# Kernel tuning notes

Hardware: AMD Instinct MI355X
Metric: run time of the kernel (lower is better)

The kernel has to match this reference:

```python
import jax, jax.numpy as jnp
import numpy as np

B, L, NV = 16, 512, 64
D = 512
PATCH_LEN, STRIDE, PADDING = 16, 8, 8
N_PATCH = (L - PATCH_LEN) // STRIDE + 2  # 64
PRED = 192
MEM = 8192
TOPK = 8
NHEAD = 4
NORM_CONST = 0.4
HEAD_NF = D * N_PATCH


def _pos_emb(n, d):
    pos = np.arange(n)[:, None].astype(np.float32)
    div = np.exp(np.arange(0, d, 2).astype(np.float32) * (-np.log(10000.0) / d))
    pe = np.zeros((n, d), np.float32)
    pe[:, 0::2] = np.sin(pos * div)
    pe[:, 1::2] = np.cos(pos * div)
    return jnp.asarray(pe)

POS = _pos_emb(N_PATCH, D)


def gelu(x):
    return jax.nn.gelu(x, approximate=False)  # torch nn.GELU default = exact erf


def setup_inputs() -> dict:
    key = jax.random.key(0)
    ks = jax.random.split(key, 16)
    s = lambda i, shape, scale=0.02: jax.random.normal(ks[i], shape, jnp.float32) * scale
    return dict(
        x_enc=jax.random.normal(ks[0], (B, L, NV), jnp.float32),
        W_val=s(1, (PATCH_LEN, D), 0.05),
        mem_bank=s(2, (MEM, D), 1.0),
        W_m1=s(3, (D, 2 * D)), b_m1=jnp.zeros((2 * D,), jnp.float32),
        W_m2=s(4, (2 * D, D)), b_m2=jnp.zeros((D,), jnp.float32),
        W_q=s(5, (D, D)), b_q=jnp.zeros((D,), jnp.float32),
        W_k=s(6, (D, D)), b_k=jnp.zeros((D,), jnp.float32),
        W_v=s(7, (D, D)), b_v=jnp.zeros((D,), jnp.float32),
        W_o=s(8, (D, D)), b_o=jnp.zeros((D,), jnp.float32),
        W_g1=s(9, (2 * D, D)), b_g1=jnp.zeros((D,), jnp.float32),
        W_g2=s(10, (D, 2)), b_g2=jnp.zeros((2,), jnp.float32),
        W_h=s(11, (HEAD_NF, PRED)), b_h=jnp.zeros((PRED,), jnp.float32),
        W_f1=s(12, (PRED, 2 * PRED)), b_f1=jnp.zeros((2 * PRED,), jnp.float32),
        W_f2=s(13, (2 * PRED, PRED)), b_f2=jnp.zeros((PRED,), jnp.float32),
    )


def reference(x_enc, W_val, mem_bank, W_m1, b_m1, W_m2, b_m2,
              W_q, b_q, W_k, b_k, W_v, b_v, W_o, b_o,
              W_g1, b_g1, W_g2, b_g2, W_h, b_h, W_f1, b_f1, W_f2, b_f2):
    # instance normalization over the time axis (means detached in torch)
    means = jax.lax.stop_gradient(jnp.mean(x_enc, axis=1, keepdims=True))
    xc = x_enc - means
    stdev = jnp.sqrt(jnp.var(xc, axis=1, keepdims=True) + 1e-5) / NORM_CONST
    x = xc / stdev                                              # [B, L, NV]

    # patch embedding: replication pad at end, unfold, linear + sinusoidal pos
    xt = jnp.transpose(x, (0, 2, 1))                            # [B, NV, L]
    xt = jnp.concatenate([xt, jnp.repeat(xt[..., -1:], PADDING, axis=-1)], axis=-1)
    win = (jnp.arange(N_PATCH) * STRIDE)[:, None] + jnp.arange(PATCH_LEN)  # [N, P]
    patches = xt[..., win].reshape(B * NV, N_PATCH, PATCH_LEN)  # [BN, N, P]
    emb = patches @ W_val + POS                                 # [BN, N, D]

    # local memory: mean-pooled query -> matmul similarity -> top-k gather -> MLP
    qflat = jnp.mean(emb, axis=1)                               # [BN, D]
    sim = qflat @ mem_bank.T                                    # [BN, MEM]
    _, idx = jax.lax.top_k(sim, TOPK)                           # [BN, K]
    retr = mem_bank[idx]                                        # [BN, K, D]
    h = gelu(retr @ W_m1 + b_m1) @ W_m2 + b_m2
    local = jnp.mean(h, axis=1, keepdims=True) + emb            # [BN, N, D]

    # global memory: multihead self-attention (4 heads, batch_first)
    dh = D // NHEAD
    heads = lambda t: t.reshape(B * NV, N_PATCH, NHEAD, dh).transpose(0, 2, 1, 3)
    q = heads(emb @ W_q + b_q)
    k = heads(emb @ W_k + b_k)
    v = heads(emb @ W_v + b_v)
    att = jax.nn.softmax(jnp.einsum('bhqd,bhkd->bhqk', q, k) / jnp.sqrt(jnp.float32(dh)), axis=-1)
    glob = jnp.einsum('bhqk,bhkd->bhqd', att, v).transpose(0, 2, 1, 3).reshape(B * NV, N_PATCH, D)
    glob = glob @ W_o + b_o                                     # [BN, N, D]

    # gated fusion of local/global memory
    comb = jnp.concatenate([local, glob], axis=-1)              # [BN, N, 2D]
    gate = jax.nn.softmax(gelu(comb @ W_g1 + b_g1) @ W_g2 + b_g2, axis=-1)
    mem = gate[..., 0:1] * local + gate[..., 1:2] * glob        # [BN, N, D]

    # flatten -> memory head -> fusion layer with residual
    flat = mem.reshape(B * NV, HEAD_NF)
    mh = (flat @ W_h + b_h).reshape(B, NV, PRED)
    pred = gelu(gelu(mh @ W_f1 + b_f1) @ W_f2 + b_f2) + mh
    pred = jnp.transpose(pred, (0, 2, 1))                       # [B, PRED, NV]

    # denormalize
    return pred * stdev + means
```

## Files before the change

kernel.cpp:

```cpp
#include <hip/hip_runtime.h>
#include <stdint.h>

#define DEV __device__ __forceinline__

typedef uint16_t u16;
typedef __bf16 bf16x8 __attribute__((ext_vector_type(8)));
typedef float f32x4 __attribute__((ext_vector_type(4)));
typedef u16 u16x8 __attribute__((ext_vector_type(8)));

DEV float bf2f(u16 v) { return __uint_as_float(((uint32_t)v) << 16); }
DEV u16 f2bf(float f) {
  uint32_t u = __float_as_uint(f);
  u += 0x7fffu + ((u >> 16) & 1u);
  return (u16)(u >> 16);
}
DEV float gelu_f(float x) { return 0.5f * x * (1.0f + erff(x * 0.7071067811865475f)); }

DEV void gload_lds16(const u16* g, u16* l) {
  __builtin_amdgcn_global_load_lds(
      (const __attribute__((address_space(1))) void*)g,
      (__attribute__((address_space(3))) void*)l, 16, 0, 0);
}

struct __align__(16) Scratch {
  float POSb[64 * 512];
  float meanv[1024];
  float stdv[1024];
  float mh[1024 * 192];
  int idxB[8192];
  float qflat[1024 * 512];
  float gatel[65536 * 2];
  float bqkv[1536];
  u16 hmeanB[1024 * 512];
  u16 gmeanB[1024 * 1024];
  u16 WqkvT[1536 * 512];
  u16 WoT[512 * 512];
  u16 Wm1T[1024 * 512];
  u16 Wm2T[512 * 1024];
  u16 Wg1T[512 * 1024];
  u16 WhT[256 * 32768];
  u16 memdupB[8192 * 1536];
  u16 embh[65536 * 512];
  u16 qkvb[65536 * 1536];
};
__device__ Scratch g_s;

__global__ __launch_bounds__(256) void zerof_kernel(float* __restrict__ p, int n) {
  int t = blockIdx.x * 256 + threadIdx.x;
  if (t < n) p[t] = 0.f;
}
__global__ __launch_bounds__(256) void zerou_kernel(u16* __restrict__ p, int n) {
  int t = blockIdx.x * 256 + threadIdx.x;
  if (t < n) p[t] = 0;
}
__global__ __launch_bounds__(256) void biasqkv_kernel(const float* __restrict__ bq,
                                                      const float* __restrict__ bk,
                                                      const float* __restrict__ bv,
                                                      float* __restrict__ o) {
  int t = blockIdx.x * 256 + threadIdx.x;
  o[t] = t < 512 ? bq[t] : (t < 1024 ? bk[t - 512] : bv[t - 1024]);
}

__global__ __launch_bounds__(256) void pos_kernel(float* __restrict__ POS) {
  int n = blockIdx.x;
  int i = threadIdx.x;
  float div = expf((float)(2 * i) * (-9.210340371976184f / 512.0f));
  float arg = (float)n * div;
  POS[n * 512 + 2 * i] = sinf(arg);
  POS[n * 512 + 2 * i + 1] = cosf(arg);
}

__global__ __launch_bounds__(256) void stats_kernel(const float* __restrict__ x_enc,
                                                    float* __restrict__ meanv,
                                                    float* __restrict__ stdv) {
  int b = blockIdx.x;
  int v = threadIdx.x & 63;
  int g = threadIdx.x >> 6;
  float s = 0.f, s2 = 0.f;
  for (int l = g; l < 512; l += 4) {
    float x = x_enc[((long)b * 512 + l) * 64 + v];
    s += x; s2 += x * x;
  }
  __shared__ float sh[2][4][64];
  sh[0][g][v] = s; sh[1][g][v] = s2;
  __syncthreads();
  if (g == 0) {
    s = sh[0][0][v] + sh[0][1][v] + sh[0][2][v] + sh[0][3][v];
    s2 = sh[1][0][v] + sh[1][1][v] + sh[1][2][v] + sh[1][3][v];
    float mu = s * (1.f / 512.f);
    float var = s2 * (1.f / 512.f) - mu * mu;
    meanv[b * 64 + v] = mu;
    stdv[b * 64 + v] = sqrtf(var + 1e-5f) * 2.5f;
  }
}

__global__ __launch_bounds__(256) void transpose_kernel(const float* __restrict__ in,
                                                        u16* __restrict__ out, int R, int C) {
  __shared__ u16 t[32][33];
  int bx = blockIdx.x * 32;
  int by = blockIdx.y * 32;
  int tx = threadIdx.x & 31, ty = threadIdx.x >> 5;
  for (int i = ty; i < 32; i += 8) t[i][tx] = f2bf(in[(long)(by + i) * C + bx + tx]);
  __syncthreads();
  for (int i = ty; i < 32; i += 8) out[(long)(bx + i) * R + by + tx] = t[tx][i];
}

__global__ __launch_bounds__(256) void emb_kernel(const float* __restrict__ x_enc,
                                                  const float* __restrict__ W_val,
                                                  const float* __restrict__ POS,
                                                  const float* __restrict__ meanv,
                                                  const float* __restrict__ stdv,
                                                  u16* __restrict__ embh,
                                                  float* __restrict__ qflat) {
  int bn = blockIdx.x;
  int b = bn >> 6, v = bn & 63;
  int tid = threadIdx.x;
  __shared__ __align__(16) float wv[16 * 512];
  __shared__ __align__(16) float pt[64 * 16];
  for (int i = tid; i < 8192; i += 256) wv[i] = W_val[i];
  float mu = meanv[bn];
  float inv = 1.f / stdv[bn];
  for (int i = tid; i < 1024; i += 256) {
    int n = i >> 4, p = i & 15;
    int l = n * 8 + p; if (l > 511) l = 511;
    pt[i] = (x_enc[((long)b * 512 + l) * 64 + v] - mu) * inv;
  }
  __syncthreads();
  float qs0 = 0.f, qs1 = 0.f;
  int d0 = tid, d1 = tid + 256;
  for (int n = 0; n < 64; ++n) {
    float a0 = POS[n * 512 + d0], a1 = POS[n * 512 + d1];
#pragma unroll
    for (int p = 0; p < 16; ++p) {
      float pv = pt[n * 16 + p];
      a0 += pv * wv[p * 512 + d0];
      a1 += pv * wv[p * 512 + d1];
    }
    long base = ((long)bn * 64 + n) * 512;
    embh[base + d0] = f2bf(a0);
    embh[base + d1] = f2bf(a1);
    qs0 += a0; qs1 += a1;
  }
  qflat[(long)bn * 512 + d0] = qs0 * (1.f / 64.f);
  qflat[(long)bn * 512 + d1] = qs1 * (1.f / 64.f);
}

__global__ __launch_bounds__(256) void qsplit_kernel(const float* __restrict__ qflat,
                                                     u16* __restrict__ qsC) {
  int t = blockIdx.x * 256 + threadIdx.x;
  int bn = t >> 6, d8 = (t & 63) * 8;
  const float* src = qflat + (long)bn * 512 + d8;
  u16x8 hi, lo;
#pragma unroll
  for (int z = 0; z < 8; ++z) {
    float q = src[z];
    u16 h = f2bf(q);
    hi[z] = h;
    lo[z] = f2bf(q - bf2f(h));
  }
  long base = (long)bn * 1536 + d8;
  *(u16x8*)(qsC + base) = hi;
  *(u16x8*)(qsC + base + 512) = lo;
  *(u16x8*)(qsC + base + 1024) = hi;
}

__global__ __launch_bounds__(256) void memdup_kernel(const float* __restrict__ mb,
                                                     u16* __restrict__ md) {
  int t = blockIdx.x * 256 + threadIdx.x;
  int n = t >> 6, k8 = (t & 63) * 8;
  const float* src = mb + (long)n * 512 + k8;
  u16x8 hi, lo;
#pragma unroll
  for (int z = 0; z < 8; ++z) {
    float m = src[z];
    u16 h = f2bf(m);
    hi[z] = h;
    lo[z] = f2bf(m - bf2f(h));
  }
  long base = (long)n * 1536 + k8;
  *(u16x8*)(md + base) = hi;
  *(u16x8*)(md + base + 512) = hi;
  *(u16x8*)(md + base + 1024) = lo;
}

template <int EPI>
__global__ __launch_bounds__(256) void gemm_nt(const u16* __restrict__ Ag,
                                               const u16* __restrict__ Bt,
                                               const float* __restrict__ bias,
                                               void* __restrict__ C,
                                               int lda, int ldb, int K, int Nreal, int ldc,
                                               int nT) {
  __shared__ __align__(16) u16 smem[2 * 128 * 64];
  u16* As = smem;
  u16* Bs = smem + 8192;
  const int tid = threadIdx.x;
  const int id = blockIdx.x;
  const int xcd = id & 7;
  const int kk = id >> 3;
  const long bm = (long)((kk / nT) * 8 + xcd) * 128;
  const long bnn = (long)(kk % nT) * 128;
  const long koff = (long)blockIdx.z * K;
  const int lane = tid & 63;
  const int w = tid >> 6;
  const int wm = (w & 1) * 64;
  const int wn = (w >> 1) * 64;
  const int r16 = lane & 15;
  const int q4 = lane >> 4;

  f32x4 acc[4][4] = {};

  const u16* ap[4];
  const u16* bp[4];
  u16* al[4];
  u16* bl[4];
#pragma unroll
  for (int j = 0; j < 4; ++j) {
    int cid = (j * 4 + w) * 64 + lane;
    int r = cid >> 3;
    int g = (cid & 7) ^ (r & 7);
    ap[j] = Ag + (bm + r) * lda + koff + g * 8;
    bp[j] = Bt + (bnn + r) * ldb + koff + g * 8;
    al[j] = As + cid * 8;
    bl[j] = Bs + cid * 8;
  }

  for (int k0 = 0; k0 < K; k0 += 64) {
#pragma unroll
    for (int j = 0; j < 4; ++j) gload_lds16(ap[j] + k0, al[j]);
#pragma unroll
    for (int j = 0; j < 4; ++j) gload_lds16(bp[j] + k0, bl[j]);
    __syncthreads();
#pragma unroll
    for (int sub = 0; sub < 2; ++sub) {
      const int gg = q4 + sub * 4;
      bf16x8 av[4], bv[4];
#pragma unroll
      for (int i = 0; i < 4; ++i) {
        int r = wm + i * 16 + r16;
        av[i] = *reinterpret_cast<const bf16x8*>(As + (r * 8 + (gg ^ (r & 7))) * 8);
      }
#pragma unroll
      for (int j2 = 0; j2 < 4; ++j2) {
        int r = wn + j2 * 16 + r16;
        bv[j2] = *reinterpret_cast<const bf16x8*>(Bs + (r * 8 + (gg ^ (r & 7))) * 8);
      }
#pragma unroll
      for (int i = 0; i < 4; ++i)
#pragma unroll
        for (int j2 = 0; j2 < 4; ++j2)
          acc[i][j2] = __builtin_amdgcn_mfma_f32_16x16x32_bf16(av[i], bv[j2], acc[i][j2], 0, 0, 0);
    }
    __syncthreads();
  }

  if (EPI == 2) {
#pragma unroll
    for (int i = 0; i < 4; ++i)
#pragma unroll
      for (int j = 0; j < 4; ++j)
#pragma unroll
        for (int r = 0; r < 4; ++r) {
          long grow = bm + wm + i * 16 + q4 * 4 + r;
          int gcol = (int)bnn + wn + j * 16 + r16;
          if (gcol < Nreal) atomicAdd((float*)C + grow * ldc + gcol, acc[i][j][r]);
        }
  } else if (EPI == 3) {
    float* epf = (float*)smem + w * 2048;
#pragma unroll
    for (int half = 0; half < 2; ++half) {
#pragma unroll
      for (int i = 0; i < 2; ++i)
#pragma unroll
        for (int j = 0; j < 4; ++j)
#pragma unroll
          for (int r = 0; r < 4; ++r)
            epf[(i * 16 + q4 * 4 + r) * 64 + j * 16 + r16] = acc[half * 2 + i][j][r];
      __syncthreads();
#pragma unroll
      for (int v2 = 0; v2 < 8; ++v2) {
        int idx = v2 * 64 + lane;
        int row = idx >> 4, c4 = (idx & 15) * 4;
        f32x4 vec = *(const f32x4*)(epf + row * 64 + c4);
        long grow = bm + wm + half * 32 + row;
        int gcol = (int)bnn + wn + c4;
        if (gcol < Nreal) *(f32x4*)((float*)C + grow * (long)ldc + gcol) = vec;
      }
      __syncthreads();
    }
  } else {
    u16* ep = smem + w * 4096;
    float bcol[4];
#pragma unroll
    for (int j = 0; j < 4; ++j) bcol[j] = bias[bnn + wn + j * 16 + r16];
#pragma unroll
    for (int i = 0; i < 4; ++i)
#pragma unroll
      for (int j = 0; j < 4; ++j)
#pragma unroll
        for (int r = 0; r < 4; ++r) {
          float v = acc[i][j][r] + bcol[j];
          if (EPI == 1) v = gelu_f(v);
          ep[(i * 16 + q4 * 4 + r) * 64 + j * 16 + r16] = f2bf(v);
        }
    __syncthreads();
#pragma unroll
    for (int v2 = 0; v2 < 8; ++v2) {
      int row = v2 * 8 + (lane >> 3);
      int c8 = (lane & 7) * 8;
      u16x8 vec = *(const u16x8*)(ep + row * 64 + c8);
      long grow = bm + wm + row;
      int gcol = (int)bnn + wn + c8;
      if (gcol < Nreal) *(u16x8*)((u16*)C + grow * (long)ldc + gcol) = vec;
    }
  }
}

DEV bool better(float v1, int i1, float v2, int i2) {
  return v1 > v2 || (v1 == v2 && i1 < i2);
}
__global__ __launch_bounds__(256) void topk_kernel(const float* __restrict__ sim,
                                                   int* __restrict__ idxout) {
  const int bn = blockIdx.x;
  const int tid = threadIdx.x;
  const float* row = sim + (long)bn * 8192;
  float bv[8]; int bi[8];
#pragma unroll
  for (int r = 0; r < 8; ++r) { bv[r] = -3.0e38f; bi[r] = 0x7fffffff; }
  for (int n = tid; n < 8192; n += 256) {
    float v = row[n];
    if (better(v, n, bv[7], bi[7])) {
      bv[7] = v; bi[7] = n;
      for (int r = 7; r > 0; --r) {
        if (!better(bv[r], bi[r], bv[r - 1], bi[r - 1])) break;
        float tv = bv[r]; bv[r] = bv[r - 1]; bv[r - 1] = tv;
        int ti = bi[r]; bi[r] = bi[r - 1]; bi[r - 1] = ti;
      }
    }
  }
  __shared__ float lv[256 * 8];
  __shared__ int li[256 * 8];
#pragma unroll
  for (int r = 0; r < 8; ++r) { lv[tid * 8 + r] = bv[r]; li[tid * 8 + r] = bi[r]; }
  __syncthreads();
  for (int step = 128; step >= 1; step >>= 1) {
    if (tid < step) {
      float av[8], xv[8]; int ai[8], xi[8];
#pragma unroll
      for (int r = 0; r < 8; ++r) {
        av[r] = lv[tid * 8 + r]; ai[r] = li[tid * 8 + r];
        xv[r] = lv[(tid + step) * 8 + r]; xi[r] = li[(tid + step) * 8 + r];
      }
      int ia = 0, ib = 0;
      float mv[8]; int mi[8];
#pragma unroll
      for (int r = 0; r < 8; ++r) {
        if (better(av[ia], ai[ia], xv[ib], xi[ib])) { mv[r] = av[ia]; mi[r] = ai[ia]; ++ia; }
        else { mv[r] = xv[ib]; mi[r] = xi[ib]; ++ib; }
      }
#pragma unroll
      for (int r = 0; r < 8; ++r) { lv[tid * 8 + r] = mv[r]; li[tid * 8 + r] = mi[r]; }
    }
    __syncthreads();
  }
  if (tid < 8) idxout[bn * 8 + tid] = li[tid];
}

__global__ __launch_bounds__(256) void gather_kernel(const float* __restrict__ mb,
                                                     const int* __restrict__ idx,
                                                     u16* __restrict__ retrB) {
  int t = blockIdx.x * 256 + threadIdx.x;
  int m = t >> 6;
  int c8 = (t & 63) * 8;
  long r = idx[m];
  if (r < 0) r = 0;
  if (r > 8191) r = 8191;
  const float* src = mb + r * 512 + c8;
  u16x8 o;
#pragma unroll
  for (int z = 0; z < 8; ++z) o[z] = f2bf(src[z]);
  *(u16x8*)(retrB + (long)m * 512 + c8) = o;
}

__global__ __launch_bounds__(256) void gmean_kernel(const u16* __restrict__ hid,
                                                    u16* __restrict__ gmeanB) {
  int t = blockIdx.x * 256 + threadIdx.x;
  int bn = t >> 7, j8 = (t & 127) * 8;
  float s[8] = {};
#pragma unroll
  for (int k = 0; k < 8; ++k) {
    u16x8 v = *(const u16x8*)(hid + (long)(bn * 8 + k) * 1024 + j8);
#pragma unroll
    for (int z = 0; z < 8; ++z) s[z] += bf2f(v[z]);
  }
  u16x8 o;
#pragma unroll
  for (int z = 0; z < 8; ++z) o[z] = f2bf(s[z] * 0.125f);
  *(u16x8*)(gmeanB + (long)bn * 1024 + j8) = o;
}

__global__ __launch_bounds__(256) void attn_kernel(u16* __restrict__ qkvb) {
  __shared__ __align__(16) u16 smem[26752];
  u16* Qs = smem;
  u16* Ks = smem + 8704;
  float* ss = (float*)(smem + 8704);
  u16* ps = smem;
  u16* Vb = smem + 17408;
  float* red = (float*)(smem + 25728);
  const int bn = blockIdx.x, h = blockIdx.y;
  const int tid = threadIdx.x;
  const int lane = tid & 63, w = tid >> 6;
  const int r16 = lane & 15, q4 = lane >> 4;
  const long base = (long)bn * 64 * 1536 + h * 128;

  for (int c = tid; c < 1024; c += 256) {
    int r = c >> 4, c8 = (c & 15) * 8;
    u16x8 vq = *(const u16x8*)(qkvb + base + (long)r * 1536 + c8);
    u16x8 vk = *(const u16x8*)(qkvb + base + (long)r * 1536 + 512 + c8);
    u16x8 vv = *(const u16x8*)(qkvb + base + (long)r * 1536 + 1024 + c8);
    *(u16x8*)(Qs + r * 136 + c8) = vq;
    *(u16x8*)(Ks + r * 136 + c8) = vk;
    int kt = r >> 5, q4t = (r >> 3) & 3, e = r & 7;
    int nt = c8 >> 4, rb = c8 & 15;
    int vbase = (nt * 2 + kt) * 520 + (q4t * 16 + rb) * 8 + e;
#pragma unroll
    for (int z = 0; z < 8; ++z) Vb[vbase + z * 8] = vv[z];
  }
  __syncthreads();

  const int m0 = w * 16;
  f32x4 accS[4] = {};
#pragma unroll
  for (int k0 = 0; k0 < 128; k0 += 32) {
    bf16x8 av = *(const bf16x8*)(Qs + (m0 + r16) * 136 + k0 + q4 * 8);
#pragma unroll
    for (int j = 0; j < 4; ++j) {
      bf16x8 bvf = *(const bf16x8*)(Ks + (j * 16 + r16) * 136 + k0 + q4 * 8);
      accS[j] = __builtin_amdgcn_mfma_f32_16x16x32_bf16(av, bvf, accS[j], 0, 0, 0);
    }
  }
  __syncthreads();
  const float scale = 0.08838834764831845f;
#pragma unroll
  for (int j = 0; j < 4; ++j)
#pragma unroll
    for (int r = 0; r < 4; ++r)
      ss[(m0 + q4 * 4 + r) * 66 + j * 16 + r16] = accS[j][r] * scale;
  __syncthreads();

  {
    int r = tid >> 2, p = tid & 3;
    float* row = ss + r * 66 + p * 16;
    float mx = -3.0e38f;
#pragma unroll
    for (int c2 = 0; c2 < 16; ++c2) mx = fmaxf(mx, row[c2]);
    red[r * 4 + p] = mx;
    __syncthreads();
    float m4 = fmaxf(fmaxf(red[r * 4], red[r * 4 + 1]),
                     fmaxf(red[r * 4 + 2], red[r * 4 + 3]));
    float s = 0.f;
#pragma unroll
    for (int c2 = 0; c2 < 16; ++c2) {
      float e = expf(row[c2] - m4);
      row[c2] = e;
      s += e;
    }
    red[256 + r * 4 + p] = s;
    __syncthreads();
    float inv = 1.f / (red[256 + r * 4] + red[256 + r * 4 + 1] +
                       red[256 + r * 4 + 2] + red[256 + r * 4 + 3]);
    u16x8 o0, o1;
#pragma unroll
    for (int z = 0; z < 8; ++z) {
      o0[z] = f2bf(row[z] * inv);
      o1[z] = f2bf(row[8 + z] * inv);
    }
    *(u16x8*)(ps + r * 72 + p * 16) = o0;
    *(u16x8*)(ps + r * 72 + p * 16 + 8) = o1;
  }
  __syncthreads();

  bf16x8 av0 = *(const bf16x8*)(ps + (m0 + r16) * 72 + q4 * 8);
  bf16x8 av1 = *(const bf16x8*)(ps + (m0 + r16) * 72 + 32 + q4 * 8);
#pragma unroll
  for (int nt = 0; nt < 8; ++nt) {
    f32x4 accO = {};
    bf16x8 bv0 = *(const bf16x8*)(Vb + (nt * 2 + 0) * 520 + lane * 8);
    bf16x8 bv1 = *(const bf16x8*)(Vb + (nt * 2 + 1) * 520 + lane * 8);
    accO = __builtin_amdgcn_mfma_f32_16x16x32_bf16(av0, bv0, accO, 0, 0, 0);
    accO = __builtin_amdgcn_mfma_f32_16x16x32_bf16(av1, bv1, accO, 0, 0, 0);
    int d = nt * 16 + r16;
#pragma unroll
    for (int r = 0; r < 4; ++r) {
      int i = m0 + q4 * 4 + r;
      qkvb[base + (long)i * 1536 + d] = f2bf(accO[r]);
    }
  }
}

__global__ __launch_bounds__(256) void local_kernel(u16* __restrict__ embh,
                                                    const u16* __restrict__ hmeanB) {
  long t = (long)blockIdx.x * 256 + threadIdx.x;
  long e8 = t * 8;
  long m = e8 >> 9;
  int d = (int)(e8 & 511);
  int bn = (int)(m >> 6);
  u16x8 a = *(const u16x8*)(embh + e8);
  u16x8 b = *(const u16x8*)(hmeanB + (long)bn * 512 + d);
  u16x8 o;
#pragma unroll
  for (int z = 0; z < 8; ++z) o[z] = f2bf(bf2f(a[z]) + bf2f(b[z]));
  *(u16x8*)(embh + e8) = o;
}

__global__ __launch_bounds__(256) void gemm_cat(const u16* __restrict__ A1,
                                                const u16* __restrict__ A2,
                                                const u16* __restrict__ Bt,
                                                const float* __restrict__ bias,
                                                const float* __restrict__ W_g2,
                                                float* __restrict__ gatel,
                                                int lda1, int lda2, int nT) {
  __shared__ __align__(16) u16 smem[2 * 128 * 64];
  u16* As = smem;
  u16* Bs = smem + 8192;
  const int tid = threadIdx.x;
  const int id = blockIdx.x;
  const int xcd = id & 7;
  const int kk = id >> 3;
  const long bm = (long)((kk / nT) * 8 + xcd) * 128;
  const long bnn = (long)(kk % nT) * 128;
  const int lane = tid & 63;
  const int w = tid >> 6;
  const int wm = (w & 1) * 64;
  const int wn = (w >> 1) * 64;
  const int r16 = lane & 15;
  const int q4 = lane >> 4;

  f32x4 acc[4][4] = {};

  const u16* ap1[4];
  const u16* ap2[4];
  const u16* bp[4];
  u16* al[4];
  u16* bl[4];
#pragma unroll
  for (int j = 0; j < 4; ++j) {
    int cid = (j * 4 + w) * 64 + lane;
    int r = cid >> 3;
    int g = (cid & 7) ^ (r & 7);
    ap1[j] = A1 + (bm + r) * lda1 + g * 8;
    ap2[j] = A2 + (bm + r) * lda2 + g * 8;
    bp[j] = Bt + (bnn + r) * 1024 + g * 8;
    al[j] = As + cid * 8;
    bl[j] = Bs + cid * 8;
  }

  for (int k0 = 0; k0 < 1024; k0 += 64) {
    if (k0 < 512) {
#pragma unroll
      for (int j = 0; j < 4; ++j) gload_lds16(ap1[j] + k0, al[j]);
    } else {
#pragma unroll
      for (int j = 0; j < 4; ++j) gload_lds16(ap2[j] + (k0 - 512), al[j]);
    }
#pragma unroll
    for (int j = 0; j < 4; ++j) gload_lds16(bp[j] + k0, bl[j]);
    __syncthreads();
#pragma unroll
    for (int sub = 0; sub < 2; ++sub) {
      const int gg = q4 + sub * 4;
      bf16x8 av[4], bv[4];
#pragma unroll
      for (int i = 0; i < 4; ++i) {
        int r = wm + i * 16 + r16;
        av[i] = *reinterpret_cast<const bf16x8*>(As + (r * 8 + (gg ^ (r & 7))) * 8);
      }
#pragma unroll
      for (int j2 = 0; j2 < 4; ++j2) {
        int r = wn + j2 * 16 + r16;
        bv[j2] = *reinterpret_cast<const bf16x8*>(Bs + (r * 8 + (gg ^ (r & 7))) * 8);
      }
#pragma unroll
      for (int i = 0; i < 4; ++i)
#pragma unroll
        for (int j2 = 0; j2 < 4; ++j2)
          acc[i][j2] = __builtin_amdgcn_mfma_f32_16x16x32_bf16(av[i], bv[j2], acc[i][j2], 0, 0, 0);
    }
    __syncthreads();
  }

  float bcol[4], w0[4], w1[4];
#pragma unroll
  for (int j = 0; j < 4; ++j) {
    int gc = (int)bnn + wn + j * 16 + r16;
    bcol[j] = bias[gc];
    w0[j] = W_g2[gc * 2];
    w1[j] = W_g2[gc * 2 + 1];
  }
#pragma unroll
  for (int i = 0; i < 4; ++i)
#pragma unroll
    for (int r = 0; r < 4; ++r) {
      float a0 = 0.f, a1 = 0.f;
#pragma unroll
      for (int j = 0; j < 4; ++j) {
        float h = gelu_f(acc[i][j][r] + bcol[j]);
        a0 += h * w0[j];
        a1 += h * w1[j];
      }
#pragma unroll
      for (int off = 1; off < 16; off <<= 1) {
        a0 += __shfl_xor(a0, off);
        a1 += __shfl_xor(a1, off);
      }
      if (r16 == 0) {
        long row = bm + wm + i * 16 + q4 * 4 + r;
        atomicAdd(&gatel[row * 2], a0);
        atomicAdd(&gatel[row * 2 + 1], a1);
      }
    }
}

__global__ __launch_bounds__(256) void memc_kernel(u16* __restrict__ embh,
                                                   const u16* __restrict__ qkvb,
                                                   const float* __restrict__ gatel,
                                                   const float* __restrict__ b_g2) {
  long t = (long)blockIdx.x * 256 + threadIdx.x;
  long e8 = t * 8;
  long m = e8 >> 9;
  int d = (int)(e8 & 511);
  float l0 = gatel[m * 2] + b_g2[0];
  float l1 = gatel[m * 2 + 1] + b_g2[1];
  float mx = fmaxf(l0, l1);
  float e0 = expf(l0 - mx), e1 = expf(l1 - mx);
  float inv = 1.f / (e0 + e1);
  float g0 = e0 * inv, g1 = e1 * inv;
  u16x8 loc = *(const u16x8*)(embh + e8);
  u16x8 gl = *(const u16x8*)(qkvb + m * 1536 + 512 + d);
  u16x8 o;
#pragma unroll
  for (int z = 0; z < 8; ++z) o[z] = f2bf(g0 * bf2f(loc[z]) + g1 * bf2f(gl[z]));
  *(u16x8*)(embh + e8) = o;
}

__global__ __launch_bounds__(256) void fusion_kernel(const float* __restrict__ mh,
                                                     const float* __restrict__ b_h,
                                                     const float* __restrict__ W_f1,
                                                     const float* __restrict__ b_f1,
                                                     const float* __restrict__ W_f2,
                                                     const float* __restrict__ b_f2,
                                                     const float* __restrict__ meanv,
                                                     const float* __restrict__ stdv,
                                                     float* __restrict__ out) {
  int bn = blockIdx.x;
  int tid = threadIdx.x;
  __shared__ float mrow[192];
  __shared__ float h1[384];
  if (tid < 192) mrow[tid] = mh[(long)bn * 192 + tid] + b_h[tid];
  __syncthreads();
  for (int j = tid; j < 384; j += 256) {
    float a = b_f1[j];
    for (int i = 0; i < 192; ++i) a += mrow[i] * W_f1[i * 384 + j];
    h1[j] = gelu_f(a);
  }
  __syncthreads();
  if (tid < 192) {
    float a = b_f2[tid];
    for (int j = 0; j < 384; ++j) a += h1[j] * W_f2[j * 192 + tid];
    float o = gelu_f(a) + mrow[tid];
    int b = bn >> 6, v = bn & 63;
    out[((long)b * 192 + tid) * 64 + v] = o * stdv[bn] + meanv[bn];
  }
}

extern "C" void kernel_launch(void* const* d_in, const int* in_sizes, int n_in,
                              void* d_out, int out_size, void* d_ws, size_t ws_size,
                              hipStream_t stream) {
  (void)in_sizes; (void)n_in; (void)out_size; (void)d_ws; (void)ws_size;
  const float* x_enc = (const float*)d_in[0];
  const float* W_val = (const float*)d_in[1];
  const float* mem_bank = (const float*)d_in[2];
  const float* W_m1 = (const float*)d_in[3];
  const float* b_m1 = (const float*)d_in[4];
  const float* W_m2 = (const float*)d_in[5];
  const float* b_m2 = (const float*)d_in[6];
  const float* W_q = (const float*)d_in[7];
  const float* b_q = (const float*)d_in[8];
  const float* W_k = (const float*)d_in[9];
  const float* b_k = (const float*)d_in[10];
  const float* W_v = (const float*)d_in[11];
  const float* b_v = (const float*)d_in[12];
  const float* W_o = (const float*)d_in[13];
  const float* b_o = (const float*)d_in[14];
  const float* W_g1 = (const float*)d_in[15];
  const float* b_g1 = (const float*)d_in[16];
  const float* W_g2 = (const float*)d_in[17];
  const float* b_g2 = (const float*)d_in[18];
  const float* W_h = (const float*)d_in[19];
  const float* b_h = (const float*)d_in[20];
  const float* W_f1 = (const float*)d_in[21];
  const float* b_f1 = (const float*)d_in[22];
  const float* W_f2 = (const float*)d_in[23];
  const float* b_f2 = (const float*)d_in[24];

  void* sp = nullptr;
  hipGetSymbolAddress(&sp, HIP_SYMBOL(g_s));
  Scratch* S = (Scratch*)sp;
  float* simB = (float*)S->qkvb;
  u16* qsC = S->qkvb + (size_t)16 * 1024 * 1024;
  u16* retrB = S->qkvb + (size_t)18 * 1024 * 1024;
  u16* hiddenB = S->qkvb + (size_t)24 * 1024 * 1024;

  pos_kernel<<<64, 256, 0, stream>>>(S->POSb);
  stats_kernel<<<16, 256, 0, stream>>>(x_enc, S->meanv, S->stdv);
  zerof_kernel<<<768, 256, 0, stream>>>(S->mh, 1024 * 192);
  zerof_kernel<<<512, 256, 0, stream>>>(S->gatel, 65536 * 2);
  zerou_kernel<<<8192, 256, 0, stream>>>(S->WhT + (size_t)192 * 32768, 64 * 32768);
  biasqkv_kernel<<<6, 256, 0, stream>>>(b_q, b_k, b_v, S->bqkv);
  transpose_kernel<<<dim3(16, 16), 256, 0, stream>>>(W_q, S->WqkvT, 512, 512);
  transpose_kernel<<<dim3(16, 16), 256, 0, stream>>>(W_k, S->WqkvT + 512 * 512, 512, 512);
  transpose_kernel<<<dim3(16, 16), 256, 0, stream>>>(W_v, S->WqkvT + 2 * 512 * 512, 512, 512);
  transpose_kernel<<<dim3(16, 16), 256, 0, stream>>>(W_o, S->WoT, 512, 512);
  transpose_kernel<<<dim3(32, 16), 256, 0, stream>>>(W_m1, S->Wm1T, 512, 1024);
  transpose_kernel<<<dim3(16, 32), 256, 0, stream>>>(W_m2, S->Wm2T, 1024, 512);
  transpose_kernel<<<dim3(16, 32), 256, 0, stream>>>(W_g1, S->Wg1T, 1024, 512);
  transpose_kernel<<<dim3(6, 1024), 256, 0, stream>>>(W_h, S->WhT, 32768, 192);
  memdup_kernel<<<2048, 256, 0, stream>>>(mem_bank, S->memdupB);

  emb_kernel<<<1024, 256, 0, stream>>>(x_enc, W_val, S->POSb, S->meanv, S->stdv,
                                       S->embh, S->qflat);
  qsplit_kernel<<<256, 256, 0, stream>>>(S->qflat, qsC);
  gemm_nt<3><<<512, 256, 0, stream>>>(qsC, S->memdupB, nullptr, simB,
                                      1536, 1536, 1536, 8192, 8192, 64);
  topk_kernel<<<1024, 256, 0, stream>>>(simB, S->idxB);
  gather_kernel<<<2048, 256, 0, stream>>>(mem_bank, S->idxB, retrB);
  gemm_nt<1><<<512, 256, 0, stream>>>(retrB, S->Wm1T, b_m1, hiddenB,
                                      512, 512, 512, 1024, 1024, 8);
  gmean_kernel<<<512, 256, 0, stream>>>(hiddenB, S->gmeanB);
  gemm_nt<0><<<32, 256, 0, stream>>>(S->gmeanB, S->Wm2T, b_m2, S->hmeanB,
                                     1024, 1024, 1024, 512, 512, 4);
  gemm_nt<0><<<6144, 256, 0, stream>>>(S->embh, S->WqkvT, S->bqkv, S->qkvb,
                                       512, 512, 512, 1536, 1536, 12);
  local_kernel<<<16384, 256, 0, stream>>>(S->embh, S->hmeanB);
  attn_kernel<<<dim3(1024, 4), 256, 0, stream>>>(S->qkvb);
  gemm_nt<0><<<2048, 256, 0, stream>>>(S->qkvb, S->WoT, b_o, S->qkvb + 512,
                                       1536, 512, 512, 512, 1536, 4);
  gemm_cat<<<2048, 256, 0, stream>>>(S->embh, S->qkvb + 512, S->Wg1T, b_g1,
                                     W_g2, S->gatel, 512, 1536, 4);
  memc_kernel<<<16384, 256, 0, stream>>>(S->embh, S->qkvb, S->gatel, b_g2);
  gemm_nt<2><<<dim3(16, 1, 16), 256, 0, stream>>>(S->embh, S->WhT, nullptr, S->mh,
                                                  32768, 32768, 2048, 192, 192, 2);
  fusion_kernel<<<1024, 256, 0, stream>>>(S->mh, b_h, W_f1, b_f1, W_f2, b_f2,
                                          S->meanv, S->stdv, (float*)d_out);
}
```

Before: 985.7 us.

## Replace split-K atomics with partial buffers, swizzle epilogue LDS, coalesce attention output

The head GEMM's split-K reduction moves off float atomicAdd. Each of the 16 K-slices now writes its own partial buffer (reusing qkvb scratch), and the fusion kernel sums the 16 partials. This also drops the zeroing of mh. GEMM epilogue LDS staging gets an XOR swizzle to avoid bank conflicts, attention output is staged through LDS so global stores are coalesced 16-byte writes, and the WhT zero-fill kernel is vectorised. Costs are extra partial-buffer traffic and added syncs in attention.

```diff
diff --git a/kernel.cpp b/kernel.cpp
--- a/kernel.cpp
+++ b/kernel.cpp
@@ -49,9 +49,9 @@
   int t = blockIdx.x * 256 + threadIdx.x;
   if (t < n) p[t] = 0.f;
 }
-__global__ __launch_bounds__(256) void zerou_kernel(u16* __restrict__ p, int n) {
+__global__ __launch_bounds__(256) void zerou8_kernel(u16* __restrict__ p, int n8) {
   int t = blockIdx.x * 256 + threadIdx.x;
-  if (t < n) p[t] = 0;
+  if (t < n8) *(u16x8*)(p + (long)t * 8) = (u16x8)0;
 }
 __global__ __launch_bounds__(256) void biasqkv_kernel(const float* __restrict__ bq,
                                                       const float* __restrict__ bk,
@@ -189,7 +189,7 @@
                                                const float* __restrict__ bias,
                                                void* __restrict__ C,
                                                int lda, int ldb, int K, int Nreal, int ldc,
-                                               int nT) {
+                                               int nT, long zstride) {
   __shared__ __align__(16) u16 smem[2 * 128 * 64];
   u16* As = smem;
   u16* Bs = smem + 8192;
@@ -253,18 +253,8 @@
     __syncthreads();
   }
 
-  if (EPI == 2) {
-#pragma unroll
-    for (int i = 0; i < 4; ++i)
-#pragma unroll
-      for (int j = 0; j < 4; ++j)
-#pragma unroll
-        for (int r = 0; r < 4; ++r) {
-          long grow = bm + wm + i * 16 + q4 * 4 + r;
-          int gcol = (int)bnn + wn + j * 16 + r16;
-          if (gcol < Nreal) atomicAdd((float*)C + grow * ldc + gcol, acc[i][j][r]);
-        }
-  } else if (EPI == 3) {
+  if (EPI == 3) {
+    float* Cz = (float*)C + (long)blockIdx.z * zstride;
     float* epf = (float*)smem + w * 2048;
 #pragma unroll
     for (int half = 0; half < 2; ++half) {
@@ -274,16 +264,18 @@
         for (int j = 0; j < 4; ++j)
 #pragma unroll
           for (int r = 0; r < 4; ++r)
-            epf[(i * 16 + q4 * 4 + r) * 64 + j * 16 + r16] = acc[half * 2 + i][j][r];
+            epf[(i * 16 + q4 * 4 + r) * 64 + ((j * 16 + r16) ^ (q4 << 4))] =
+                acc[half * 2 + i][j][r];
       __syncthreads();
 #pragma unroll
       for (int v2 = 0; v2 < 8; ++v2) {
         int idx = v2 * 64 + lane;
         int row = idx >> 4, c4 = (idx & 15) * 4;
-        f32x4 vec = *(const f32x4*)(epf + row * 64 + c4);
+        int c4s = c4 ^ (((row >> 2) & 3) << 4);
+        f32x4 vec = *(const f32x4*)(epf + row * 64 + c4s);
         long grow = bm + wm + half * 32 + row;
         int gcol = (int)bnn + wn + c4;
-        if (gcol < Nreal) *(f32x4*)((float*)C + grow * (long)ldc + gcol) = vec;
+        if (gcol < Nreal) *(f32x4*)(Cz + grow * (long)ldc + gcol) = vec;
       }
       __syncthreads();
     }
@@ -300,14 +292,15 @@
         for (int r = 0; r < 4; ++r) {
           float v = acc[i][j][r] + bcol[j];
           if (EPI == 1) v = gelu_f(v);
-          ep[(i * 16 + q4 * 4 + r) * 64 + j * 16 + r16] = f2bf(v);
+          ep[(i * 16 + q4 * 4 + r) * 64 + ((j * 16 + r16) ^ (q4 << 4))] = f2bf(v);
         }
     __syncthreads();
 #pragma unroll
     for (int v2 = 0; v2 < 8; ++v2) {
       int row = v2 * 8 + (lane >> 3);
       int c8 = (lane & 7) * 8;
-      u16x8 vec = *(const u16x8*)(ep + row * 64 + c8);
+      int c8s = c8 ^ (((row >> 2) & 3) << 4);
+      u16x8 vec = *(const u16x8*)(ep + row * 64 + c8s);
       long grow = bm + wm + row;
       int gcol = (int)bnn + wn + c8;
       if (gcol < Nreal) *(u16x8*)((u16*)C + grow * (long)ldc + gcol) = vec;
@@ -404,6 +397,7 @@
   u16* Ks = smem + 8704;
   float* ss = (float*)(smem + 8704);
   u16* ps = smem;
+  u16* Os = smem;
   u16* Vb = smem + 17408;
   float* red = (float*)(smem + 25728);
   const int bn = blockIdx.x, h = blockIdx.y;
@@ -481,6 +475,7 @@
 
   bf16x8 av0 = *(const bf16x8*)(ps + (m0 + r16) * 72 + q4 * 8);
   bf16x8 av1 = *(const bf16x8*)(ps + (m0 + r16) * 72 + 32 + q4 * 8);
+  __syncthreads();
 #pragma unroll
   for (int nt = 0; nt < 8; ++nt) {
     f32x4 accO = {};
@@ -488,12 +483,21 @@
     bf16x8 bv1 = *(const bf16x8*)(Vb + (nt * 2 + 1) * 520 + lane * 8);
     accO = __builtin_amdgcn_mfma_f32_16x16x32_bf16(av0, bv0, accO, 0, 0, 0);
     accO = __builtin_amdgcn_mfma_f32_16x16x32_bf16(av1, bv1, accO, 0, 0, 0);
-    int d = nt * 16 + r16;
 #pragma unroll
     for (int r = 0; r < 4; ++r) {
       int i = m0 + q4 * 4 + r;
-      qkvb[base + (long)i * 1536 + d] = f2bf(accO[r]);
-    }
+      int col = nt * 16 + r16;
+      Os[i * 128 + (col ^ (q4 << 4))] = f2bf(accO[r]);
+    }
+  }
+  __syncthreads();
+#pragma unroll
+  for (int z = 0; z < 4; ++z) {
+    int idx = z * 256 + tid;
+    int row = idx >> 4, c8 = (idx & 15) * 8;
+    int c8s = c8 ^ (((row >> 2) & 3) << 4);
+    u16x8 vec = *(const u16x8*)(Os + row * 128 + c8s);
+    *(u16x8*)(qkvb + base + (long)row * 1536 + c8) = vec;
   }
 }
 
@@ -642,7 +646,7 @@
   *(u16x8*)(embh + e8) = o;
 }
 
-__global__ __launch_bounds__(256) void fusion_kernel(const float* __restrict__ mh,
+__global__ __launch_bounds__(256) void fusion_kernel(const float* __restrict__ mh16,
                                                      const float* __restrict__ b_h,
                                                      const float* __restrict__ W_f1,
                                                      const float* __restrict__ b_f1,
@@ -655,7 +659,12 @@
   int tid = threadIdx.x;
   __shared__ float mrow[192];
   __shared__ float h1[384];
-  if (tid < 192) mrow[tid] = mh[(long)bn * 192 + tid] + b_h[tid];
+  if (tid < 192) {
+    float a = b_h[tid];
+#pragma unroll
+    for (int z = 0; z < 16; ++z) a += mh16[(long)z * 196608 + (long)bn * 192 + tid];
+    mrow[tid] = a;
+  }
   __syncthreads();
   for (int j = tid; j < 384; j += 256) {
     float a = b_f1[j];
@@ -709,12 +718,12 @@
   u16* qsC = S->qkvb + (size_t)16 * 1024 * 1024;
   u16* retrB = S->qkvb + (size_t)18 * 1024 * 1024;
   u16* hiddenB = S->qkvb + (size_t)24 * 1024 * 1024;
+  float* mh16 = (float*)S->qkvb;
 
   pos_kernel<<<64, 256, 0, stream>>>(S->POSb);
   stats_kernel<<<16, 256, 0, stream>>>(x_enc, S->meanv, S->stdv);
-  zerof_kernel<<<768, 256, 0, stream>>>(S->mh, 1024 * 192);
   zerof_kernel<<<512, 256, 0, stream>>>(S->gatel, 65536 * 2);
-  zerou_kernel<<<8192, 256, 0, stream>>>(S->WhT + (size_t)192 * 32768, 64 * 32768);
+  zerou8_kernel<<<1024, 256, 0, stream>>>(S->WhT + (size_t)192 * 32768, 64 * 32768 / 8);
   biasqkv_kernel<<<6, 256, 0, stream>>>(b_q, b_k, b_v, S->bqkv);
   transpose_kernel<<<dim3(16, 16), 256, 0, stream>>>(W_q, S->WqkvT, 512, 512);
   transpose_kernel<<<dim3(16, 16), 256, 0, stream>>>(W_k, S->WqkvT + 512 * 512, 512, 512);
@@ -730,25 +739,26 @@
                                        S->embh, S->qflat);
   qsplit_kernel<<<256, 256, 0, stream>>>(S->qflat, qsC);
   gemm_nt<3><<<512, 256, 0, stream>>>(qsC, S->memdupB, nullptr, simB,
-                                      1536, 1536, 1536, 8192, 8192, 64);
+                                      1536, 1536, 1536, 8192, 8192, 64, 0L);
   topk_kernel<<<1024, 256, 0, stream>>>(simB, S->idxB);
   gather_kernel<<<2048, 256, 0, stream>>>(mem_bank, S->idxB, retrB);
   gemm_nt<1><<<512, 256, 0, stream>>>(retrB, S->Wm1T, b_m1, hiddenB,
-                                      512, 512, 512, 1024, 1024, 8);
+                                      512, 512, 512, 1024, 1024, 8, 0L);
   gmean_kernel<<<512, 256, 0, stream>>>(hiddenB, S->gmeanB);
   gemm_nt<0><<<32, 256, 0, stream>>>(S->gmeanB, S->Wm2T, b_m2, S->hmeanB,
-                                     1024, 1024, 1024, 512, 512, 4);
+                                     1024, 1024, 1024, 512, 512, 4, 0L);
   gemm_nt<0><<<6144, 256, 0, stream>>>(S->embh, S->WqkvT, S->bqkv, S->qkvb,
-                                       512, 512, 512, 1536, 1536, 12);
+                                       512, 512, 512, 1536, 1536, 12, 0L);
   local_kernel<<<16384, 256, 0, stream>>>(S->embh, S->hmeanB);
   attn_kernel<<<dim3(1024, 4), 256, 0, stream>>>(S->qkvb);
   gemm_nt<0><<<2048, 256, 0, stream>>>(S->qkvb, S->WoT, b_o, S->qkvb + 512,
-                                       1536, 512, 512, 512, 1536, 4);
+                                       1536, 512, 512, 512, 1536, 4, 0L);
   gemm_cat<<<2048, 256, 0, stream>>>(S->embh, S->qkvb + 512, S->Wg1T, b_g1,
                                      W_g2, S->gatel, 512, 1536, 4);
   memc_kernel<<<16384, 256, 0, stream>>>(S->embh, S->qkvb, S->gatel, b_g2);
-  gemm_nt<2><<<dim3(16, 1, 16), 256, 0, stream>>>(S->embh, S->WhT, nullptr, S->mh,
-                                                  32768, 32768, 2048, 192, 192, 2);
-  fusion_kernel<<<1024, 256, 0, stream>>>(S->mh, b_h, W_f1, b_f1, W_f2, b_f2,
+  gemm_nt<3><<<dim3(16, 1, 16), 256, 0, stream>>>(S->embh, S->WhT, nullptr, mh16,
+                                                  32768, 32768, 2048, 192, 192, 2,
+                                                  196608L);
+  fusion_kernel<<<1024, 256, 0, stream>>>(mh16, b_h, W_f1, b_f1, W_f2, b_f2,
                                           S->meanv, S->stdv, (float*)d_out);
 }
```

After: 1.008 ms. +2.2%, slower.
